# Performance work log

Measured on AMD Instinct MI355X. Metric: run time of the kernel, lower is better.

## Reference

```python
import jax, jax.numpy as jnp
import numpy as np

N_NODES = 100000


def gcn_conv(x, src, dst, ew, W, b, n):
    """PyG GCNConv: self-loops (weight 1), symmetric norm, linear + bias.
    src/dst/ew already include self-loops."""
    xw = x @ W  # [N, out]
    deg = jax.ops.segment_sum(ew, dst, num_segments=n)  # in-degree with weights
    dinv = jnp.where(deg > 0, jax.lax.rsqrt(deg), 0.0)
    norm = dinv[src] * ew * dinv[dst]  # [E]
    msgs = xw[src] * norm[:, None]  # gather + scale
    out = jax.ops.segment_sum(msgs, dst, num_segments=n)  # scatter-add
    return out + b


def setup_inputs() -> dict:
    key = jax.random.key(0)
    k1, k2, k3, k4, k5 = jax.random.split(key, 5)
    x = jax.random.normal(k1, (N_NODES, 512), dtype=jnp.float32)
    edge_index = jax.random.randint(k2, (2, 3200000), 0, N_NODES, dtype=jnp.int64)
    edge_weight = jax.random.uniform(k3, (3200000,), dtype=jnp.float32)
    W1 = jax.random.normal(k4, (512, 64), dtype=jnp.float32) * (1.0 / np.sqrt(512))
    b1 = jnp.zeros((64,), dtype=jnp.float32)
    W2 = jax.random.normal(k5, (64, 20), dtype=jnp.float32) * (1.0 / np.sqrt(64))
    b2 = jnp.zeros((20,), dtype=jnp.float32)
    return {"x": x, "edge_index": edge_index, "edge_weight": edge_weight,
            "W1": W1, "b1": b1, "W2": W2, "b2": b2}


def reference(x, edge_index, edge_weight, W1, b1, W2, b2):
    n = x.shape[0]
    loops = jnp.arange(n, dtype=edge_index.dtype)
    src = jnp.concatenate([edge_index[0], loops])
    dst = jnp.concatenate([edge_index[1], loops])
    ew = jnp.concatenate([edge_weight, jnp.ones((n,), dtype=edge_weight.dtype)])
    h = gcn_conv(x, src, dst, ew, W1, b1, n)
    h = jax.nn.relu(h)  # dropout is identity in eval mode
    h = gcn_conv(h, src, dst, ew, W2, b2, n)
    return jax.nn.softmax(h, axis=-1)
```

## Files before the change

kernel.cpp:

```cpp
#include <hip/hip_runtime.h>
#include <hip/hip_fp16.h>
#include <math.h>

#define FIN 512
#define H   64
#define C   20
#define CP  32

typedef _Float16 half8 __attribute__((ext_vector_type(8)));
typedef float floatx4 __attribute__((ext_vector_type(4)));

__device__ __forceinline__ int detect_m64(const int* __restrict__ ei) {
    int nz = 0;
    #pragma unroll
    for (int i = 0; i < 32; i++) nz |= ei[2 * i + 1];
    return nz == 0;
}

__device__ __forceinline__ int edge_val(const int* __restrict__ ei, long long idx, int m64) {
    return m64 ? ei[2 * idx] : ei[(int)idx];
}

__global__ void init_kernel(const float* __restrict__ W, _Float16* __restrict__ W1T,
                            unsigned long long* __restrict__ packed, int N) {
    int tid = blockIdx.x * 256 + threadIdx.x;
    if (tid < H * FIN) {
        int n = tid >> 9, k = tid & 511;
        W1T[tid] = (_Float16)W[k * H + n];
    }
    if (tid < N) packed[tid] = 0ULL;
}

#define FIXSCALE 268435456.0f
#define KC 64
#define GM 64
#define HE 2048
__global__ __launch_bounds__(256, 8) void fused_gemm1_hist_kernel(
        const float* __restrict__ x, const _Float16* __restrict__ W1T,
        __half* __restrict__ xwh, int N,
        const int* __restrict__ ei, const float* __restrict__ ew,
        unsigned long long* __restrict__ packed, int* __restrict__ rankdst,
        int E, int GB, int HB) {
    __shared__ _Float16 xsh[GM][72];
    __shared__ _Float16 wsh[64][72];

    int nb = blockIdx.x;
    int minB = (GB < HB) ? GB : HB;
    int isHist, roleId;
    if (nb < 2 * minB) { isHist = !(nb & 1); roleId = nb >> 1; }
    else { int r = nb - 2 * minB; isHist = (HB > GB); roleId = minB + r; }

    if (isHist) {
        int m64 = detect_m64(ei);
        long long base = (long long)roleId * HE + threadIdx.x;
        int d[8]; float w[8];
        #pragma unroll
        for (int u = 0; u < 8; u++) {
            long long e = base + u * 256;
            if (e < E) { d[u] = edge_val(ei, (long long)E + e, m64); w[u] = ew[e]; }
            else d[u] = -1;
        }
        unsigned long long old[8];
        #pragma unroll
        for (int u = 0; u < 8; u++)
            if (d[u] >= 0) {
                unsigned long long add = (1ULL << 40) |
                    (unsigned long long)(w[u] * FIXSCALE + 0.5f);
                old[u] = atomicAdd(&packed[d[u]], add);
            }
        #pragma unroll
        for (int u = 0; u < 8; u++)
            if (d[u] >= 0)
                rankdst[base + u * 256] = ((int)(old[u] >> 40) << 17) | d[u];
        return;
    }

    int tid  = threadIdx.x;
    int wave = tid >> 6;
    int lane = tid & 63;
    int quad = lane >> 4;
    int l16  = lane & 15;
    int row0 = roleId * GM;

    floatx4 acc[4];
    #pragma unroll
    for (int ct = 0; ct < 4; ct++) acc[ct] = (floatx4){0.f, 0.f, 0.f, 0.f};

    int col4  = (tid & 15) * 4;
    int rbase = tid >> 4;
    int wn = tid >> 2;
    int wk = (tid & 3) * 16;

    for (int k0 = 0; k0 < FIN; k0 += KC) {
        #pragma unroll
        for (int it = 0; it < 4; it++) {
            int row = rbase + it * 16;
            int grow = row0 + row; if (grow >= N) grow = N - 1;
            float4 v = *(const float4*)&x[(long long)grow * FIN + k0 + col4];
            _Float16* p = &xsh[row][col4];
            p[0] = (_Float16)v.x; p[1] = (_Float16)v.y;
            p[2] = (_Float16)v.z; p[3] = (_Float16)v.w;
        }
        *(half8*)&wsh[wn][wk]     = *(const half8*)&W1T[wn * FIN + k0 + wk];
        *(half8*)&wsh[wn][wk + 8] = *(const half8*)&W1T[wn * FIN + k0 + wk + 8];
        __syncthreads();
        #pragma unroll
        for (int kk = 0; kk < KC; kk += 32) {
            half8 a0 = *(const half8*)&xsh[wave * 16 + l16][kk + quad * 8];
            #pragma unroll
            for (int ct = 0; ct < 4; ct++) {
                half8 b = *(const half8*)&wsh[ct * 16 + l16][kk + quad * 8];
                acc[ct] = __builtin_amdgcn_mfma_f32_16x16x32_f16(a0, b, acc[ct], 0, 0, 0);
            }
        }
        __syncthreads();
    }
    #pragma unroll
    for (int ct = 0; ct < 4; ct++)
        #pragma unroll
        for (int r = 0; r < 4; r++) {
            int grow = row0 + wave * 16 + quad * 4 + r;
            if (grow < N)
                xwh[(long long)grow * H + ct * 16 + l16] = __float2half(acc[ct][r]);
        }
}

__global__ void block_sums_kernel(const unsigned long long* __restrict__ packed,
                                  int* __restrict__ bsum, int N) {
    __shared__ int lds[256];
    int t = threadIdx.x;
    int base = blockIdx.x * 1024 + t * 4;
    int s = 0;
    #pragma unroll
    for (int k = 0; k < 4; k++) { int i = base + k; if (i < N) s += (int)(packed[i] >> 40); }
    lds[t] = s; __syncthreads();
    for (int off = 128; off > 0; off >>= 1) {
        if (t < off) lds[t] += lds[t + off];
        __syncthreads();
    }
    if (t == 0) bsum[blockIdx.x] = lds[0];
}

__global__ void scan_local_kernel(const unsigned long long* __restrict__ packed,
                                  const int* __restrict__ bsum,
                                  int* __restrict__ rowptr, float* __restrict__ dinv,
                                  int N, int E) {
    __shared__ int lds[256];
    int t = threadIdx.x, bid = blockIdx.x;
    lds[t] = (t < bid) ? bsum[t] : 0;
    __syncthreads();
    for (int off = 128; off > 0; off >>= 1) {
        if (t < off) lds[t] += lds[t + off];
        __syncthreads();
    }
    int bpre = lds[0];
    __syncthreads();

    int base = bid * 1024 + t * 4;
    int c[4]; int s = 0;
    #pragma unroll
    for (int k = 0; k < 4; k++) {
        int i = base + k;
        if (i < N) {
            unsigned long long v = packed[i];
            c[k] = (int)(v >> 40);
            dinv[i] = rsqrtf((float)(v & ((1ULL << 40) - 1)) * (1.0f / FIXSCALE) + 1.0f);
        } else c[k] = 0;
        s += c[k];
    }
    lds[t] = s; __syncthreads();
    for (int off = 1; off < 256; off <<= 1) {
        int add = (t >= off) ? lds[t - off] : 0;
        __syncthreads();
        lds[t] += add;
        __syncthreads();
    }
    int start = bpre + lds[t] - s;
    #pragma unroll
    for (int k = 0; k < 4; k++) {
        int i = base + k;
        if (i < N) { rowptr[i] = start; start += c[k]; }
    }
    if (bid == 0 && t == 0) rowptr[N] = E;
}

__global__ void fill2_kernel(const int* __restrict__ ei, const float* __restrict__ ew,
                             const int* __restrict__ rowptr,
                             const int* __restrict__ rankdst, int2* __restrict__ edata, int E) {
    int m64 = detect_m64(ei);
    long long t = (long long)blockIdx.x * blockDim.x + threadIdx.x;
    long long e0 = 2 * t;
    if (e0 >= E) return;
    int s0, s1;
    if (m64) {
        int4 sp = *(const int4*)&ei[2 * e0];
        s0 = sp.x; s1 = sp.z;
    } else {
        int2 sp = *(const int2*)&ei[e0];
        s0 = sp.x; s1 = sp.y;
    }
    float2 w = *(const float2*)&ew[e0];
    int2  rd = *(const int2*)&rankdst[e0];
    int d0 = rd.x & 131071, rk0 = rd.x >> 17;
    int d1 = rd.y & 131071, rk1 = rd.y >> 17;
    edata[rowptr[d0] + rk0] = make_int2(s0, __float_as_int(w.x));
    if (e0 + 1 < E)
        edata[rowptr[d1] + rk1] = make_int2(s1, __float_as_int(w.y));
}

#define A1_NODES 8
__global__ __launch_bounds__(256) void agg1g2_kernel(
        const int* __restrict__ rowptr, const int2* __restrict__ edata,
        const __half* __restrict__ xwh, const float* __restrict__ dinv,
        const float* __restrict__ b1, const float* __restrict__ W2,
        __half* __restrict__ zp, int N) {
    __shared__ float hs[A1_NODES][H + 2];
    __shared__ float w2s[H * C];
    for (int t = threadIdx.x; t < H * C; t += 256) w2s[t] = W2[t];
    int hw = threadIdx.x >> 5;
    int l  = threadIdx.x & 31;
    int i  = blockIdx.x * A1_NODES + hw;
    if (i < N) {
        int start = rowptr[i], end = rowptr[i + 1];
        float a0 = 0.f, a1 = 0.f;
        int j = start;
        for (; j + 3 < end; j += 4) {
            int2 e0 = edata[j], e1 = edata[j + 1], e2 = edata[j + 2], e3 = edata[j + 3];
            float ds0 = dinv[e0.x], ds1 = dinv[e1.x], ds2 = dinv[e2.x], ds3 = dinv[e3.x];
            float2 v0 = __half22float2(*(const __half2*)&xwh[(long long)e0.x * H + 2 * l]);
            float2 v1 = __half22float2(*(const __half2*)&xwh[(long long)e1.x * H + 2 * l]);
            float2 v2 = __half22float2(*(const __half2*)&xwh[(long long)e2.x * H + 2 * l]);
            float2 v3 = __half22float2(*(const __half2*)&xwh[(long long)e3.x * H + 2 * l]);
            float n0 = __int_as_float(e0.y) * ds0, n1 = __int_as_float(e1.y) * ds1;
            float n2 = __int_as_float(e2.y) * ds2, n3 = __int_as_float(e3.y) * ds3;
            a0 = fmaf(v0.x, n0, a0); a1 = fmaf(v0.y, n0, a1);
            a0 = fmaf(v1.x, n1, a0); a1 = fmaf(v1.y, n1, a1);
            a0 = fmaf(v2.x, n2, a0); a1 = fmaf(v2.y, n2, a1);
            a0 = fmaf(v3.x, n3, a0); a1 = fmaf(v3.y, n3, a1);
        }
        for (; j < end; j++) {
            int2 e0 = edata[j];
            float2 v0 = __half22float2(*(const __half2*)&xwh[(long long)e0.x * H + 2 * l]);
            float n0 = __int_as_float(e0.y) * dinv[e0.x];
            a0 = fmaf(v0.x, n0, a0); a1 = fmaf(v0.y, n0, a1);
        }
        float di = dinv[i];
        float2 vs = __half22float2(*(const __half2*)&xwh[(long long)i * H + 2 * l]);
        a0 = fmaf(vs.x, di, a0); a1 = fmaf(vs.y, di, a1);
        float2 bb = *(const float2*)&b1[2 * l];
        hs[hw][2 * l]     = fmaxf(fmaf(a0, di, bb.x), 0.f);
        hs[hw][2 * l + 1] = fmaxf(fmaf(a1, di, bb.y), 0.f);
    }
    __syncthreads();
    int r = threadIdx.x >> 5, c = threadIdx.x & 31;
    int node = blockIdx.x * A1_NODES + r;
    if (node < N) {
        float v = 0.f;
        if (c < C) {
            float acc = 0.f;
            #pragma unroll
            for (int k = 0; k < H; k++) acc = fmaf(hs[r][k], w2s[k * C + c], acc);
            v = acc * dinv[node];
        }
        zp[(long long)node * CP + c] = __float2half(v);
    }
}

__global__ void agg2_final_kernel(const int* __restrict__ rowptr, const int2* __restrict__ edata,
                                  const __half* __restrict__ zp, const float* __restrict__ dinv,
                                  const float* __restrict__ b2, float* __restrict__ out, int N) {
    long long gid = (long long)blockIdx.x * blockDim.x + threadIdx.x;
    int wid = (int)(gid >> 6);
    int half = (threadIdx.x & 63) >> 5;
    int l = threadIdx.x & 31;
    int i = wid * 2 + half;
    float acc = 0.f;
    bool active = (i < N) && (l < C);
    if (active) {
        int start = rowptr[i], end = rowptr[i + 1];
        int j = start;
        for (; j + 3 < end; j += 4) {
            int2 e0 = edata[j], e1 = edata[j + 1], e2 = edata[j + 2], e3 = edata[j + 3];
            float v0 = __half2float(zp[(long long)e0.x * CP + l]);
            float v1 = __half2float(zp[(long long)e1.x * CP + l]);
            float v2 = __half2float(zp[(long long)e2.x * CP + l]);
            float v3 = __half2float(zp[(long long)e3.x * CP + l]);
            acc = fmaf(v0, __int_as_float(e0.y), acc);
            acc = fmaf(v1, __int_as_float(e1.y), acc);
            acc = fmaf(v2, __int_as_float(e2.y), acc);
            acc = fmaf(v3, __int_as_float(e3.y), acc);
        }
        for (; j < end; j++) {
            int2 e = edata[j];
            acc = fmaf(__half2float(zp[(long long)e.x * CP + l]), __int_as_float(e.y), acc);
        }
        acc += __half2float(zp[(long long)i * CP + l]);
        acc = fmaf(acc, dinv[i], b2[l]);
    }
    float v = active ? acc : -1e30f;
    float mx = v;
    #pragma unroll
    for (int off = 16; off >= 1; off >>= 1) mx = fmaxf(mx, __shfl_xor(mx, off, 32));
    float ex = active ? expf(v - mx) : 0.f;
    float sm = ex;
    #pragma unroll
    for (int off = 16; off >= 1; off >>= 1) sm += __shfl_xor(sm, off, 32);
    if (active) out[(long long)i * C + l] = ex / sm;
}

static inline size_t align256(size_t x) { return (x + 255) & ~(size_t)255; }

extern "C" void kernel_launch(void* const* d_in, const int* in_sizes, int n_in,
                              void* d_out, int out_size, void* d_ws, size_t ws_size,
                              hipStream_t stream) {
    const float* x  = (const float*)d_in[0];
    const int*   ei = (const int*)d_in[1];
    const float* ew = (const float*)d_in[2];
    const float* W1 = (const float*)d_in[3];
    const float* b1 = (const float*)d_in[4];
    const float* W2 = (const float*)d_in[5];
    const float* b2 = (const float*)d_in[6];
    float* out = (float*)d_out;

    int N = in_sizes[0] / FIN;
    int E = in_sizes[2];
    int NB = (N + 1023) / 1024;

    char* ws = (char*)d_ws;
    size_t off = 0;
    unsigned long long* packed = (unsigned long long*)(ws + off); off = align256(off + (size_t)N * 8);
    float*    dinv    = (float*)(ws + off);    off = align256(off + (size_t)N * 4);
    int*      bsum    = (int*)(ws + off);      off = align256(off + (size_t)NB * 4);
    int*      rowptr  = (int*)(ws + off);      off = align256(off + (size_t)(N + 1) * 4);
    int2*     edata   = (int2*)(ws + off);     off = align256(off + (size_t)E * 8);
    _Float16* W1T     = (_Float16*)(ws + off); off = align256(off + (size_t)H * FIN * 2);
    __half*   xw1h    = (__half*)(ws + off);   off = align256(off + (size_t)N * H * 2);
    int*      rankdst = (int*)(ws + off);      off = align256(off + (size_t)E * 4);
    __half*   zp      = (__half*)(ws + off);   off = align256(off + (size_t)N * CP * 2);

    int initBlocks = (max(H * FIN, N) + 255) / 256;
    init_kernel<<<initBlocks, 256, 0, stream>>>(W1, W1T, packed, N);

    int GB = (N + GM - 1) / GM;
    int HB = (E + HE - 1) / HE;
    fused_gemm1_hist_kernel<<<GB + HB, 256, 0, stream>>>(
        x, W1T, xw1h, N, ei, ew, packed, rankdst, E, GB, HB);

    block_sums_kernel<<<NB, 256, 0, stream>>>(packed, bsum, N);
    scan_local_kernel<<<NB, 256, 0, stream>>>(packed, bsum, rowptr, dinv, N, E);

    fill2_kernel<<<(int)(((long long)(E + 1) / 2 + 255) / 256), 256, 0, stream>>>(
        ei, ew, rowptr, rankdst, edata, E);

    agg1g2_kernel<<<(N + A1_NODES - 1) / A1_NODES, 256, 0, stream>>>(
        rowptr, edata, xw1h, dinv, b1, W2, zp, N);

    int waves2 = (N + 1) / 2;
    agg2_final_kernel<<<(int)(((long long)waves2 * 64 + 255) / 256), 256, 0, stream>>>(
        rowptr, edata, zp, dinv, b2, out, N);
}
```

Before: 636.4 us.

## Pre-scale layer-1 features by source dinv and unroll gathers by eight

GEMM1 now writes fp32 output, and a new scale_kernel multiplies each row by its dinv and stores fp16. This removes the per-edge dinv[src] gather from the layer-1 aggregation. Both aggregation loops are unrolled to eight edges to keep more gathers in flight. Workspace buffers are aliased (fp32 xw with edata, rankdst with zp) to save memory, at the cost of an extra kernel and an fp32 round-trip of the GEMM output.

```diff
diff --git a/kernel.cpp b/kernel.cpp
--- a/kernel.cpp
+++ b/kernel.cpp
@@ -37,7 +37,7 @@
 #define HE 2048
 __global__ __launch_bounds__(256, 8) void fused_gemm1_hist_kernel(
         const float* __restrict__ x, const _Float16* __restrict__ W1T,
-        __half* __restrict__ xwh, int N,
+        float* __restrict__ xw1f, int N,
         const int* __restrict__ ei, const float* __restrict__ ew,
         unsigned long long* __restrict__ packed, int* __restrict__ rankdst,
         int E, int GB, int HB) {
@@ -121,7 +121,7 @@
         for (int r = 0; r < 4; r++) {
             int grow = row0 + wave * 16 + quad * 4 + r;
             if (grow < N)
-                xwh[(long long)grow * H + ct * 16 + l16] = __float2half(acc[ct][r]);
+                xw1f[(long long)grow * H + ct * 16 + l16] = acc[ct][r];
         }
 }
 
@@ -182,6 +182,23 @@
         if (i < N) { rowptr[i] = start; start += c[k]; }
     }
     if (bid == 0 && t == 0) rowptr[N] = E;
+}
+
+__global__ void scale_kernel(const float* __restrict__ xw1f, const float* __restrict__ dinv,
+                             _Float16* __restrict__ xws, int N) {
+    long long t = (long long)blockIdx.x * 256 + threadIdx.x;
+    if (t >= (long long)N * 8) return;
+    int i  = (int)(t >> 3);
+    int fo = ((int)t & 7) * 8;
+    float di = dinv[i];
+    const float4* p = (const float4*)&xw1f[(long long)i * H + fo];
+    float4 v0 = p[0], v1 = p[1];
+    half8 o;
+    o[0] = (_Float16)(v0.x * di); o[1] = (_Float16)(v0.y * di);
+    o[2] = (_Float16)(v0.z * di); o[3] = (_Float16)(v0.w * di);
+    o[4] = (_Float16)(v1.x * di); o[5] = (_Float16)(v1.y * di);
+    o[6] = (_Float16)(v1.z * di); o[7] = (_Float16)(v1.w * di);
+    *(half8*)&xws[(long long)i * H + fo] = o;
 }
 
 __global__ void fill2_kernel(const int* __restrict__ ei, const float* __restrict__ ew,
@@ -211,55 +228,68 @@
 #define A1_NODES 8
 __global__ __launch_bounds__(256) void agg1g2_kernel(
         const int* __restrict__ rowptr, const int2* __restrict__ edata,
-        const __half* __restrict__ xwh, const float* __restrict__ dinv,
+        const _Float16* __restrict__ xws, const float* __restrict__ dinv,
         const float* __restrict__ b1, const float* __restrict__ W2,
         __half* __restrict__ zp, int N) {
     __shared__ float hs[A1_NODES][H + 2];
     __shared__ float w2s[H * C];
     for (int t = threadIdx.x; t < H * C; t += 256) w2s[t] = W2[t];
-    int hw = threadIdx.x >> 5;
-    int l  = threadIdx.x & 31;
-    int i  = blockIdx.x * A1_NODES + hw;
+    __syncthreads();
+
+    int wv   = threadIdx.x >> 6;
+    int slot = threadIdx.x >> 5;
+    int l    = threadIdx.x & 31;
+    int i    = blockIdx.x * A1_NODES + slot;
     if (i < N) {
         int start = rowptr[i], end = rowptr[i + 1];
         float a0 = 0.f, a1 = 0.f;
         int j = start;
-        for (; j + 3 < end; j += 4) {
-            int2 e0 = edata[j], e1 = edata[j + 1], e2 = edata[j + 2], e3 = edata[j + 3];
-            float ds0 = dinv[e0.x], ds1 = dinv[e1.x], ds2 = dinv[e2.x], ds3 = dinv[e3.x];
-            float2 v0 = __half22float2(*(const __half2*)&xwh[(long long)e0.x * H + 2 * l]);
-            float2 v1 = __half22float2(*(const __half2*)&xwh[(long long)e1.x * H + 2 * l]);
-            float2 v2 = __half22float2(*(const __half2*)&xwh[(long long)e2.x * H + 2 * l]);
-            float2 v3 = __half22float2(*(const __half2*)&xwh[(long long)e3.x * H + 2 * l]);
-            float n0 = __int_as_float(e0.y) * ds0, n1 = __int_as_float(e1.y) * ds1;
-            float n2 = __int_as_float(e2.y) * ds2, n3 = __int_as_float(e3.y) * ds3;
+        for (; j + 7 < end; j += 8) {
+            int2 e0 = edata[j],     e1 = edata[j + 1], e2 = edata[j + 2], e3 = edata[j + 3];
+            int2 e4 = edata[j + 4], e5 = edata[j + 5], e6 = edata[j + 6], e7 = edata[j + 7];
+            float2 v0 = __half22float2(*(const __half2*)&xws[(long long)e0.x * H + 2 * l]);
+            float2 v1 = __half22float2(*(const __half2*)&xws[(long long)e1.x * H + 2 * l]);
+            float2 v2 = __half22float2(*(const __half2*)&xws[(long long)e2.x * H + 2 * l]);
+            float2 v3 = __half22float2(*(const __half2*)&xws[(long long)e3.x * H + 2 * l]);
+            float2 v4 = __half22float2(*(const __half2*)&xws[(long long)e4.x * H + 2 * l]);
+            float2 v5 = __half22float2(*(const __half2*)&xws[(long long)e5.x * H + 2 * l]);
+            float2 v6 = __half22float2(*(const __half2*)&xws[(long long)e6.x * H + 2 * l]);
+            float2 v7 = __half22float2(*(const __half2*)&xws[(long long)e7.x * H + 2 * l]);
+            float n0 = __int_as_float(e0.y), n1 = __int_as_float(e1.y);
+            float n2 = __int_as_float(e2.y), n3 = __int_as_float(e3.y);
+            float n4 = __int_as_float(e4.y), n5 = __int_as_float(e5.y);
+            float n6 = __int_as_float(e6.y), n7 = __int_as_float(e7.y);
             a0 = fmaf(v0.x, n0, a0); a1 = fmaf(v0.y, n0, a1);
             a0 = fmaf(v1.x, n1, a0); a1 = fmaf(v1.y, n1, a1);
             a0 = fmaf(v2.x, n2, a0); a1 = fmaf(v2.y, n2, a1);
             a0 = fmaf(v3.x, n3, a0); a1 = fmaf(v3.y, n3, a1);
+            a0 = fmaf(v4.x, n4, a0); a1 = fmaf(v4.y, n4, a1);
+            a0 = fmaf(v5.x, n5, a0); a1 = fmaf(v5.y, n5, a1);
+            a0 = fmaf(v6.x, n6, a0); a1 = fmaf(v6.y, n6, a1);
+            a0 = fmaf(v7.x, n7, a0); a1 = fmaf(v7.y, n7, a1);
         }
         for (; j < end; j++) {
             int2 e0 = edata[j];
-            float2 v0 = __half22float2(*(const __half2*)&xwh[(long long)e0.x * H + 2 * l]);
-            float n0 = __int_as_float(e0.y) * dinv[e0.x];
+            float2 v0 = __half22float2(*(const __half2*)&xws[(long long)e0.x * H + 2 * l]);
+            float n0 = __int_as_float(e0.y);
             a0 = fmaf(v0.x, n0, a0); a1 = fmaf(v0.y, n0, a1);
         }
+        float2 vs = __half22float2(*(const __half2*)&xws[(long long)i * H + 2 * l]);
+        a0 += vs.x; a1 += vs.y;
         float di = dinv[i];
-        float2 vs = __half22float2(*(const __half2*)&xwh[(long long)i * H + 2 * l]);
-        a0 = fmaf(vs.x, di, a0); a1 = fmaf(vs.y, di, a1);
         float2 bb = *(const float2*)&b1[2 * l];
-        hs[hw][2 * l]     = fmaxf(fmaf(a0, di, bb.x), 0.f);
-        hs[hw][2 * l + 1] = fmaxf(fmaf(a1, di, bb.y), 0.f);
-    }
-    __syncthreads();
-    int r = threadIdx.x >> 5, c = threadIdx.x & 31;
-    int node = blockIdx.x * A1_NODES + r;
+        hs[slot][2 * l]     = fmaxf(fmaf(a0, di, bb.x), 0.f);
+        hs[slot][2 * l + 1] = fmaxf(fmaf(a1, di, bb.y), 0.f);
+    }
+    int node_slot = wv * 2 + ((threadIdx.x & 63) >> 5);
+    int c = threadIdx.x & 31;
+    int node = blockIdx.x * A1_NODES + node_slot;
     if (node < N) {
         float v = 0.f;
         if (c < C) {
             float acc = 0.f;
             #pragma unroll
-            for (int k = 0; k < H; k++) acc = fmaf(hs[r][k], w2s[k * C + c], acc);
+            for (int k = 0; k < H; k++) acc = fmaf(hs[node_slot][k], w2s[k * C + c], acc);
             v = acc * dinv[node];
         }
         zp[(long long)node * CP + c] = __float2half(v);
@@ -279,16 +309,25 @@
     if (active) {
         int start = rowptr[i], end = rowptr[i + 1];
         int j = start;
-        for (; j + 3 < end; j += 4) {
-            int2 e0 = edata[j], e1 = edata[j + 1], e2 = edata[j + 2], e3 = edata[j + 3];
+        for (; j + 7 < end; j += 8) {
+            int2 e0 = edata[j],     e1 = edata[j + 1], e2 = edata[j + 2], e3 = edata[j + 3];
+            int2 e4 = edata[j + 4], e5 = edata[j + 5], e6 = edata[j + 6], e7 = edata[j + 7];
             float v0 = __half2float(zp[(long long)e0.x * CP + l]);
             float v1 = __half2float(zp[(long long)e1.x * CP + l]);
             float v2 = __half2float(zp[(long long)e2.x * CP + l]);
             float v3 = __half2float(zp[(long long)e3.x * CP + l]);
+            float v4 = __half2float(zp[(long long)e4.x * CP + l]);
+            float v5 = __half2float(zp[(long long)e5.x * CP + l]);
+            float v6 = __half2float(zp[(long long)e6.x * CP + l]);
+            float v7 = __half2float(zp[(long long)e7.x * CP + l]);
             acc = fmaf(v0, __int_as_float(e0.y), acc);
             acc = fmaf(v1, __int_as_float(e1.y), acc);
             acc = fmaf(v2, __int_as_float(e2.y), acc);
             acc = fmaf(v3, __int_as_float(e3.y), acc);
+            acc = fmaf(v4, __int_as_float(e4.y), acc);
+            acc = fmaf(v5, __int_as_float(e5.y), acc);
+            acc = fmaf(v6, __int_as_float(e6.y), acc);
+            acc = fmaf(v7, __int_as_float(e7.y), acc);
         }
         for (; j < end; j++) {
             int2 e = edata[j];
@@ -332,11 +371,13 @@
     float*    dinv    = (float*)(ws + off);    off = align256(off + (size_t)N * 4);
     int*      bsum    = (int*)(ws + off);      off = align256(off + (size_t)NB * 4);
     int*      rowptr  = (int*)(ws + off);      off = align256(off + (size_t)(N + 1) * 4);
-    int2*     edata   = (int2*)(ws + off);     off = align256(off + (size_t)E * 8);
+    size_t sharedSz = (size_t)E * 8 > (size_t)N * H * 4 ? (size_t)E * 8 : (size_t)N * H * 4;
+    float* xw1f  = (float*)(ws + off);
+    int2*  edata = (int2*)(ws + off);          off = align256(off + sharedSz);
     _Float16* W1T     = (_Float16*)(ws + off); off = align256(off + (size_t)H * FIN * 2);
-    __half*   xw1h    = (__half*)(ws + off);   off = align256(off + (size_t)N * H * 2);
-    int*      rankdst = (int*)(ws + off);      off = align256(off + (size_t)E * 4);
-    __half*   zp      = (__half*)(ws + off);   off = align256(off + (size_t)N * CP * 2);
+    _Float16* xws     = (_Float16*)(ws + off); off = align256(off + (size_t)N * H * 2);
+    int*    rankdst = (int*)(ws + off);
+    __half* zp      = (__half*)(ws + off);     off = align256(off + (size_t)E * 4);
 
     int initBlocks = (max(H * FIN, N) + 255) / 256;
     init_kernel<<<initBlocks, 256, 0, stream>>>(W1, W1T, packed, N);
@@ -344,16 +385,19 @@
     int GB = (N + GM - 1) / GM;
     int HB = (E + HE - 1) / HE;
     fused_gemm1_hist_kernel<<<GB + HB, 256, 0, stream>>>(
-        x, W1T, xw1h, N, ei, ew, packed, rankdst, E, GB, HB);
+        x, W1T, xw1f, N, ei, ew, packed, rankdst, E, GB, HB);
 
     block_sums_kernel<<<NB, 256, 0, stream>>>(packed, bsum, N);
     scan_local_kernel<<<NB, 256, 0, stream>>>(packed, bsum, rowptr, dinv, N, E);
 
+    scale_kernel<<<(int)(((long long)N * 8 + 255) / 256), 256, 0, stream>>>(
+        xw1f, dinv, xws, N);
+
     fill2_kernel<<<(int)(((long long)(E + 1) / 2 + 255) / 256), 256, 0, stream>>>(
         ei, ew, rowptr, rankdst, edata, E);
 
     agg1g2_kernel<<<(N + A1_NODES - 1) / A1_NODES, 256, 0, stream>>>(
-        rowptr, edata, xw1h, dinv, b1, W2, zp, N);
+        rowptr, edata, xws, dinv, b1, W2, zp, N);
 
     int waves2 = (N + 1) / 2;
     agg2_final_kernel<<<(int)(((long long)waves2 * 64 + 255) / 256), 256, 0, stream>>>(
```

Measured after the change: 630.4 us. No clear change (-0.9%).
